# Optimization experiments

Hardware: AMD Instinct MI355X
Metric: run time of the kernel (lower is better)

## Reference

```python
import jax, jax.numpy as jnp
import numpy as np

EPS = 1e-20

def setup_inputs() -> dict:
    key = jax.random.key(0)
    k1, k2 = jax.random.split(key)
    x = jax.random.normal(k1, (8192, 4096), dtype=jnp.float32)
    weight = jax.random.normal(k2, (4096, 4096), dtype=jnp.float32)  # [out, in]
    return {"x": x, "weight": weight}

def reference(x, weight):
    # Binarize activations and weights with sign(v + eps), then matmul.
    xb = jnp.sign(x + EPS)
    wb = jnp.sign(weight + EPS)
    return jnp.matmul(xb, wb.T)  # [N, out]
```

## Files before the change

kernel.cpp:

```cpp
#include <hip/hip_runtime.h>
#include <stdint.h>

#define EPSF 1e-20f

typedef __attribute__((ext_vector_type(4))) int i32x4;
typedef __attribute__((ext_vector_type(8))) int i32x8;
typedef __attribute__((ext_vector_type(16))) float f32x16;


__global__ __launch_bounds__(256)
void bin_fp4_kernel(const float4* __restrict__ src, uint32_t* __restrict__ dst,
                    int n8) {
    int base = blockIdx.x * 1024 + threadIdx.x;
#pragma unroll
    for (int j = 0; j < 4; ++j) {
        int idx = base + j * 256;
        if (idx < n8) {
            float4 v0 = src[2 * idx];
            float4 v1 = src[2 * idx + 1];
            uint32_t w = 0;
            w |= ((v0.x < -EPSF) ? 0xAu : 0x2u);
            w |= ((v0.y < -EPSF) ? 0xAu : 0x2u) << 4;
            w |= ((v0.z < -EPSF) ? 0xAu : 0x2u) << 8;
            w |= ((v0.w < -EPSF) ? 0xAu : 0x2u) << 12;
            w |= ((v1.x < -EPSF) ? 0xAu : 0x2u) << 16;
            w |= ((v1.y < -EPSF) ? 0xAu : 0x2u) << 20;
            w |= ((v1.z < -EPSF) ? 0xAu : 0x2u) << 24;
            w |= ((v1.w < -EPSF) ? 0xAu : 0x2u) << 28;
            dst[idx] = w;
        }
    }
}

#define SCALE_ONE 0x7F7F7F7Fu

__global__ __launch_bounds__(512, 2)
void fp4mfma_gemm256(const char* __restrict__ x4, const char* __restrict__ w4,
                     float* __restrict__ out) {
    __shared__ char lds[2][65536];

    const int t = threadIdx.x;
    const int lane = t & 63;
    const int wave = t >> 6;
    const int wm = (wave >> 2) * 128;
    const int wn = (wave & 3) * 64;
    const int row0 = blockIdx.y * 256;
    const int col0 = blockIdx.x * 256;
    const int lrow = lane & 31;
    const int half = lane >> 5;

    const char* xbase = x4 + (size_t)row0 * 2048;
    const char* wbase = w4 + (size_t)col0 * 2048;

    int goff[4], loff[4];
#pragma unroll
    for (int j = 0; j < 4; ++j) {
        int cid = j * 512 + t;
        int crow = cid >> 3;
        int cqg = (cid & 7) ^ (crow & 7);
        goff[j] = crow * 2048 + cqg * 16;
        loff[j] = cid * 16;
    }

    f32x16 acc[4][2];
#pragma unroll
    for (int r = 0; r < 4; ++r)
#pragma unroll
        for (int c = 0; c < 2; ++c)
#pragma unroll
            for (int e = 0; e < 16; ++e) acc[r][c][e] = 0.0f;

    i32x8 a[4], b[2];
#pragma unroll
    for (int r = 0; r < 4; ++r)
#pragma unroll
        for (int e = 0; e < 8; ++e) a[r][e] = 0;
#pragma unroll
    for (int c = 0; c < 2; ++c)
#pragma unroll
        for (int e = 0; e < 8; ++e) b[c][e] = 0;

    const int laneA = (wm + lrow) * 128;
    const int laneB = (wn + lrow) * 128;

#pragma unroll
    for (int j = 0; j < 4; ++j) {
        __builtin_amdgcn_global_load_lds((const uint32_t*)(xbase + goff[j]),
                                         (uint32_t*)(&lds[0][0] + loff[j]),
                                         16, 0, 0);
        __builtin_amdgcn_global_load_lds((const uint32_t*)(wbase + goff[j]),
                                         (uint32_t*)(&lds[0][0] + 32768 + loff[j]),
                                         16, 0, 0);
    }
    __syncthreads();

    for (int kt = 0; kt < 16; ++kt) {
        const int cur = kt & 1;
        const char* curA = &lds[cur][0];
        const char* curB = &lds[cur][0] + 32768;
        char* nxt = &lds[cur ^ 1][0];
        const int kbn = (kt + 1) * 128;
        const bool stage = (kt < 15);

#pragma unroll
        for (int m = 0; m < 4; ++m) {
            if (stage) {
                __builtin_amdgcn_global_load_lds(
                    (const uint32_t*)(xbase + goff[m] + kbn),
                    (uint32_t*)(nxt + loff[m]), 16, 0, 0);
                __builtin_amdgcn_global_load_lds(
                    (const uint32_t*)(wbase + goff[m] + kbn),
                    (uint32_t*)(nxt + 32768 + loff[m]), 16, 0, 0);
            }

            const int qs16 = (((2 * m + half) ^ (lrow & 7)) << 4);
#pragma unroll
            for (int r = 0; r < 4; ++r) {
                i32x4 av = *(const i32x4*)(curA + laneA + r * 4096 + qs16);
                a[r][0] = av[0]; a[r][1] = av[1];
                a[r][2] = av[2]; a[r][3] = av[3];
            }
#pragma unroll
            for (int c = 0; c < 2; ++c) {
                i32x4 bv = *(const i32x4*)(curB + laneB + c * 4096 + qs16);
                b[c][0] = bv[0]; b[c][1] = bv[1];
                b[c][2] = bv[2]; b[c][3] = bv[3];
            }

            __builtin_amdgcn_s_setprio(1);
#pragma unroll
            for (int r = 0; r < 4; ++r)
#pragma unroll
                for (int c = 0; c < 2; ++c)
                    acc[r][c] = __builtin_amdgcn_mfma_scale_f32_32x32x64_f8f6f4(
                        a[r], b[c], acc[r][c],
                        4, 4,
                        0, SCALE_ONE,
                        0, SCALE_ONE);
            __builtin_amdgcn_s_setprio(0);
        }
        __syncthreads();
    }

#pragma unroll
    for (int r = 0; r < 4; ++r)
#pragma unroll
        for (int c = 0; c < 2; ++c)
#pragma unroll
            for (int e = 0; e < 16; ++e) {
                int rr = row0 + wm + r * 32 + (e & 3) + 8 * (e >> 2) + 4 * half;
                int cc = col0 + wn + c * 32 + lrow;
                out[(size_t)rr * 4096 + cc] = acc[r][c][e];
            }
}


__global__ __launch_bounds__(256)
void binarize_kernel(const float* __restrict__ src,
                     unsigned long long* __restrict__ dst, int n256) {
    int wave = blockIdx.x * 4 + (threadIdx.x >> 6);
    if (wave >= n256) return;
    int lane = threadIdx.x & 63;
    const float4* p = (const float4*)(src + (size_t)wave * 256);
    float4 v = p[lane];
    unsigned long long m0 = __ballot(v.x < -EPSF);
    unsigned long long m1 = __ballot(v.y < -EPSF);
    unsigned long long m2 = __ballot(v.z < -EPSF);
    unsigned long long m3 = __ballot(v.w < -EPSF);
    if (lane < 4) {
        unsigned long long m = (lane == 0) ? m0 : (lane == 1) ? m1
                             : (lane == 2) ? m2 : m3;
        dst[(size_t)wave * 4 + lane] = m;
    }
}

#define BM 128
#define BN 128
#define CHUNK_Q 8
#define NCHUNK 4
#define LDSS 9

__global__ __launch_bounds__(256, 2)
void bingemm_kernel(const uint4* __restrict__ xb, const uint4* __restrict__ wb,
                    float* __restrict__ out) {
    __shared__ uint4 xsl[BM * LDSS];
    __shared__ uint4 wsl[BN * LDSS];

    const int t  = threadIdx.x;
    const int tx = t & 15;
    const int ty = t >> 4;
    const int row0 = blockIdx.y * BM;
    const int col0 = blockIdx.x * BN;

    int acc[8][8];
#pragma unroll
    for (int a = 0; a < 8; ++a)
#pragma unroll
        for (int b = 0; b < 8; ++b) acc[a][b] = 0;

    const int srow = t >> 3;
    const int sq   = t & 7;

    for (int c = 0; c < NCHUNK; ++c) {
        __syncthreads();
#pragma unroll
        for (int k = 0; k < 4; ++k) {
            int r = srow + 32 * k;
            xsl[r * LDSS + sq] = xb[(size_t)(row0 + r) * 32 + c * CHUNK_Q + sq];
            wsl[r * LDSS + sq] = wb[(size_t)(col0 + r) * 32 + c * CHUNK_Q + sq];
        }
        __syncthreads();

#pragma unroll
        for (int q = 0; q < CHUNK_Q; ++q) {
            uint4 xq[8], wq[8];
#pragma unroll
            for (int ri = 0; ri < 8; ++ri)
                xq[ri] = xsl[(ty + 16 * ri) * LDSS + q];
#pragma unroll
            for (int cj = 0; cj < 8; ++cj)
                wq[cj] = wsl[(tx + 16 * cj) * LDSS + q];
#pragma unroll
            for (int ri = 0; ri < 8; ++ri)
#pragma unroll
                for (int cj = 0; cj < 8; ++cj) {
                    acc[ri][cj] += __builtin_popcount(xq[ri].x ^ wq[cj].x);
                    acc[ri][cj] += __builtin_popcount(xq[ri].y ^ wq[cj].y);
                    acc[ri][cj] += __builtin_popcount(xq[ri].z ^ wq[cj].z);
                    acc[ri][cj] += __builtin_popcount(xq[ri].w ^ wq[cj].w);
                }
        }
    }

#pragma unroll
    for (int ri = 0; ri < 8; ++ri) {
        size_t i = row0 + ty + 16 * ri;
#pragma unroll
        for (int cj = 0; cj < 8; ++cj) {
            int j = col0 + tx + 16 * cj;
            out[i * 4096 + j] = (float)(4096 - 2 * acc[ri][cj]);
        }
    }
}

extern "C" void kernel_launch(void* const* d_in, const int* in_sizes, int n_in,
                              void* d_out, int out_size, void* d_ws, size_t ws_size,
                              hipStream_t stream) {
    const float* x = (const float*)d_in[0];
    const float* w = (const float*)d_in[1];
    float* out = (float*)d_out;

    const int M = 8192, N = 4096, K = 4096;
    const size_t need_fp4 = ((size_t)M * K + (size_t)N * K) / 2;

    if (ws_size >= need_fp4) {
        char* x4 = (char*)d_ws;
        char* w4 = x4 + (size_t)M * K / 2;

        int n8x = (M * K) / 8;
        int n8w = (N * K) / 8;
        bin_fp4_kernel<<<n8x / 1024, 256, 0, stream>>>(
            (const float4*)x, (uint32_t*)x4, n8x);
        bin_fp4_kernel<<<n8w / 1024, 256, 0, stream>>>(
            (const float4*)w, (uint32_t*)w4, n8w);

        dim3 grid(N / 256, M / 256);
        fp4mfma_gemm256<<<grid, 512, 0, stream>>>(x4, w4, out);
    } else {
        uint32_t* xbits = (uint32_t*)d_ws;
        uint32_t* wbits = xbits + (size_t)M * (K / 32);

        binarize_kernel<<<(M * K) / 1024, 256, 0, stream>>>(
            x, (unsigned long long*)xbits, (M * K) / 256);
        binarize_kernel<<<(N * K) / 1024, 256, 0, stream>>>(
            w, (unsigned long long*)wbits, (N * K) / 256);

        dim3 grid(N / BN, M / BM);
        bingemm_kernel<<<grid, 256, 0, stream>>>(
            (const uint4*)xbits, (const uint4*)wbits, out);
    }
}
```

Baseline: 329.2 us.

## Split K-tile into two half-phases with staged async loads and partial waits

Restructures the main GEMM loop into two phases per K tile: the first computes the top half of the A rows while the first half of the next tile's loads are issued, and the second computes the bottom half while the remaining loads go out. Full __syncthreads is replaced by explicit vmcnt waits plus barriers. B fragments are kept in registers across both phases so they are read from LDS only once. The goal is finer overlap of global-to-LDS traffic with MFMA work and lower LDS read pressure, at the cost of more registers and hand-tuned wait counts that could go wrong.

```diff
diff --git a/kernel.cpp b/kernel.cpp
--- a/kernel.cpp
+++ b/kernel.cpp
@@ -52,15 +52,10 @@
     const char* xbase = x4 + (size_t)row0 * 2048;
     const char* wbase = w4 + (size_t)col0 * 2048;
 
-    int goff[4], loff[4];
-#pragma unroll
-    for (int j = 0; j < 4; ++j) {
-        int cid = j * 512 + t;
-        int crow = cid >> 3;
-        int cqg = (cid & 7) ^ (crow & 7);
-        goff[j] = crow * 2048 + cqg * 16;
-        loff[j] = cid * 16;
-    }
+    const int srow = t >> 3;
+    const int sqg  = (t & 7) ^ (srow & 7);
+    const int gsrc = srow * 2048 + sqg * 16;
+    const int gdst = t * 16;
 
     f32x16 acc[4][2];
 #pragma unroll
@@ -70,77 +65,109 @@
 #pragma unroll
             for (int e = 0; e < 16; ++e) acc[r][c][e] = 0.0f;
 
-    i32x8 a[4], b[2];
-#pragma unroll
-    for (int r = 0; r < 4; ++r)
-#pragma unroll
-        for (int e = 0; e < 8; ++e) a[r][e] = 0;
-#pragma unroll
-    for (int c = 0; c < 2; ++c)
-#pragma unroll
-        for (int e = 0; e < 8; ++e) b[c][e] = 0;
-
-    const int laneA = (wm + lrow) * 128;
-    const int laneB = (wn + lrow) * 128;
-
-#pragma unroll
-    for (int j = 0; j < 4; ++j) {
-        __builtin_amdgcn_global_load_lds((const uint32_t*)(xbase + goff[j]),
-                                         (uint32_t*)(&lds[0][0] + loff[j]),
-                                         16, 0, 0);
-        __builtin_amdgcn_global_load_lds((const uint32_t*)(wbase + goff[j]),
-                                         (uint32_t*)(&lds[0][0] + 32768 + loff[j]),
-                                         16, 0, 0);
-    }
-    __syncthreads();
+    i32x8 a8[2], b8[2];
+#pragma unroll
+    for (int r = 0; r < 2; ++r)
+#pragma unroll
+        for (int e = 0; e < 8; ++e) { a8[r][e] = 0; b8[r][e] = 0; }
+
+    int qs16[4];
+#pragma unroll
+    for (int m = 0; m < 4; ++m)
+        qs16[m] = (((2 * m + half) ^ (lrow & 7)) << 4);
+
+    const int aoff = (wm + lrow) * 128;
+    const int boff = (wn + lrow) * 128;
+
+#define ISSUE_A(buf, g, kb)                                                   \
+    __builtin_amdgcn_global_load_lds(                                         \
+        (const uint32_t*)(xbase + (g) * 131072 + gsrc + (kb)),                \
+        (uint32_t*)((buf) + (g) * 8192 + gdst), 16, 0, 0)
+#define ISSUE_B(buf, g, kb)                                                   \
+    __builtin_amdgcn_global_load_lds(                                         \
+        (const uint32_t*)(wbase + (g) * 131072 + gsrc + (kb)),                \
+        (uint32_t*)((buf) + 32768 + (g) * 8192 + gdst), 16, 0, 0)
+
+    {
+        char* b0 = &lds[0][0];
+        ISSUE_A(b0, 0, 0); ISSUE_A(b0, 2, 0); ISSUE_B(b0, 0, 0); ISSUE_B(b0, 1, 0);
+        ISSUE_B(b0, 2, 0); ISSUE_B(b0, 3, 0); ISSUE_A(b0, 1, 0); ISSUE_A(b0, 3, 0);
+    }
+
+    i32x4 bv[2][4];
 
     for (int kt = 0; kt < 16; ++kt) {
-        const int cur = kt & 1;
-        const char* curA = &lds[cur][0];
-        const char* curB = &lds[cur][0] + 32768;
-        char* nxt = &lds[cur ^ 1][0];
-        const int kbn = (kt + 1) * 128;
-        const bool stage = (kt < 15);
-
+        char* cbuf = &lds[kt & 1][0];
+        char* nbuf = &lds[(kt & 1) ^ 1][0];
+        const int kb = (kt + 1) * 128;
+        const bool st = (kt < 15);
+
+        asm volatile("s_waitcnt vmcnt(2)" ::: "memory");
+        __builtin_amdgcn_s_barrier();
+        asm volatile("" ::: "memory");
+        if (st) {
+            ISSUE_A(nbuf, 0, kb); ISSUE_A(nbuf, 2, kb);
+            ISSUE_B(nbuf, 0, kb); ISSUE_B(nbuf, 1, kb);
+        }
 #pragma unroll
         for (int m = 0; m < 4; ++m) {
-            if (stage) {
-                __builtin_amdgcn_global_load_lds(
-                    (const uint32_t*)(xbase + goff[m] + kbn),
-                    (uint32_t*)(nxt + loff[m]), 16, 0, 0);
-                __builtin_amdgcn_global_load_lds(
-                    (const uint32_t*)(wbase + goff[m] + kbn),
-                    (uint32_t*)(nxt + 32768 + loff[m]), 16, 0, 0);
-            }
-
-            const int qs16 = (((2 * m + half) ^ (lrow & 7)) << 4);
-#pragma unroll
-            for (int r = 0; r < 4; ++r) {
-                i32x4 av = *(const i32x4*)(curA + laneA + r * 4096 + qs16);
-                a[r][0] = av[0]; a[r][1] = av[1];
-                a[r][2] = av[2]; a[r][3] = av[3];
+#pragma unroll
+            for (int r = 0; r < 2; ++r) {
+                i32x4 av = *(const i32x4*)(cbuf + aoff + r * 4096 + qs16[m]);
+                a8[r][0] = av[0]; a8[r][1] = av[1];
+                a8[r][2] = av[2]; a8[r][3] = av[3];
             }
 #pragma unroll
             for (int c = 0; c < 2; ++c) {
-                i32x4 bv = *(const i32x4*)(curB + laneB + c * 4096 + qs16);
-                b[c][0] = bv[0]; b[c][1] = bv[1];
-                b[c][2] = bv[2]; b[c][3] = bv[3];
-            }
-
+                bv[c][m] = *(const i32x4*)(cbuf + 32768 + boff + c * 4096 + qs16[m]);
+                b8[c][0] = bv[c][m][0]; b8[c][1] = bv[c][m][1];
+                b8[c][2] = bv[c][m][2]; b8[c][3] = bv[c][m][3];
+            }
             __builtin_amdgcn_s_setprio(1);
 #pragma unroll
-            for (int r = 0; r < 4; ++r)
+            for (int r = 0; r < 2; ++r)
 #pragma unroll
                 for (int c = 0; c < 2; ++c)
                     acc[r][c] = __builtin_amdgcn_mfma_scale_f32_32x32x64_f8f6f4(
-                        a[r], b[c], acc[r][c],
-                        4, 4,
-                        0, SCALE_ONE,
-                        0, SCALE_ONE);
+                        a8[r], b8[c], acc[r][c],
+                        4, 4, 0, SCALE_ONE, 0, SCALE_ONE);
             __builtin_amdgcn_s_setprio(0);
         }
-        __syncthreads();
-    }
+
+        if (st) { asm volatile("s_waitcnt vmcnt(4)" ::: "memory"); }
+        else    { asm volatile("s_waitcnt vmcnt(0)" ::: "memory"); }
+        __builtin_amdgcn_s_barrier();
+        asm volatile("" ::: "memory");
+        if (st) {
+            ISSUE_B(nbuf, 2, kb); ISSUE_B(nbuf, 3, kb);
+            ISSUE_A(nbuf, 1, kb); ISSUE_A(nbuf, 3, kb);
+        }
+#pragma unroll
+        for (int m = 0; m < 4; ++m) {
+#pragma unroll
+            for (int r = 0; r < 2; ++r) {
+                i32x4 av = *(const i32x4*)(cbuf + aoff + (2 + r) * 4096 + qs16[m]);
+                a8[r][0] = av[0]; a8[r][1] = av[1];
+                a8[r][2] = av[2]; a8[r][3] = av[3];
+            }
+#pragma unroll
+            for (int c = 0; c < 2; ++c) {
+                b8[c][0] = bv[c][m][0]; b8[c][1] = bv[c][m][1];
+                b8[c][2] = bv[c][m][2]; b8[c][3] = bv[c][m][3];
+            }
+            __builtin_amdgcn_s_setprio(1);
+#pragma unroll
+            for (int r = 0; r < 2; ++r)
+#pragma unroll
+                for (int c = 0; c < 2; ++c)
+                    acc[2 + r][c] = __builtin_amdgcn_mfma_scale_f32_32x32x64_f8f6f4(
+                        a8[r], b8[c], acc[2 + r][c],
+                        4, 4, 0, SCALE_ONE, 0, SCALE_ONE);
+            __builtin_amdgcn_s_setprio(0);
+        }
+    }
+#undef ISSUE_A
+#undef ISSUE_B
 
 #pragma unroll
     for (int r = 0; r < 4; ++r)
```

New measurement: 326.2 us. Within noise of the previous version (-0.9%).
